# Kernel optimization log

Hardware: AMD Instinct MI355X
Metric: run time of the kernel (lower is better)

The kernel has to match this reference:

```python
import jax, jax.numpy as jnp
import numpy as np
from math import sqrt

D_MODEL = 1024
N_HEADS = 16
FF_MULT = 4
MAX_DIST = 512
LN_EPS = 1e-5


def layer_norm(x, g, b):
    mu = jnp.mean(x, axis=-1, keepdims=True)
    var = jnp.var(x, axis=-1, keepdims=True)
    return (x - mu) * jax.lax.rsqrt(var + LN_EPS) * g + b


def setup_inputs() -> dict:
    key = jax.random.key(0)
    ks = jax.random.split(key, 10)
    D, H, F = D_MODEL, N_HEADS, D_MODEL * FF_MULT
    s = 0.02
    return {
        "x": jax.random.normal(ks[0], (2, 2048, D), dtype=jnp.float32),
        "w_qkv": jax.random.normal(ks[1], (D, 3 * D), dtype=jnp.float32) * s,
        "b_qkv": jnp.zeros((3 * D,), jnp.float32),
        "w_out": jax.random.normal(ks[2], (D, D), dtype=jnp.float32) * s,
        "b_out": jnp.zeros((D,), jnp.float32),
        "rel_bias": jax.random.normal(ks[3], (2 * MAX_DIST + 1, H), dtype=jnp.float32) * s,
        "g1": jnp.ones((D,), jnp.float32),
        "beta1": jnp.zeros((D,), jnp.float32),
        "w1": jax.random.normal(ks[4], (D, F), dtype=jnp.float32) * s,
        "b1": jnp.zeros((F,), jnp.float32),
        "w2": jax.random.normal(ks[5], (F, D), dtype=jnp.float32) * s,
        "b2": jnp.zeros((D,), jnp.float32),
        "g2": jnp.ones((D,), jnp.float32),
        "beta2": jnp.zeros((D,), jnp.float32),
    }


def reference(x, w_qkv, b_qkv, w_out, b_out, rel_bias, g1, beta1, w1, b1, w2, b2, g2, beta2):
    B, T, D = x.shape
    H = N_HEADS
    hd = D // H
    qkv = x @ w_qkv + b_qkv                      # [B,T,3D]
    q, k, v = jnp.split(qkv, 3, axis=-1)
    # [B,H,T,hd]
    q = q.reshape(B, T, H, hd).transpose(0, 2, 1, 3)
    k = k.reshape(B, T, H, hd).transpose(0, 2, 1, 3)
    v = v.reshape(B, T, H, hd).transpose(0, 2, 1, 3)
    scores = jnp.einsum("bhqd,bhkd->bhqk", q, k) / sqrt(hd)
    # relative position bias: gather from table [2*max_dist+1, H]
    rel = jnp.clip(jnp.arange(T)[None, :] - jnp.arange(T)[:, None], -MAX_DIST, MAX_DIST) + MAX_DIST
    bias = rel_bias[rel].transpose(2, 0, 1)       # [H,T,T]
    attn = jax.nn.softmax(scores + bias[None], axis=-1)
    out = jnp.einsum("bhqk,bhkd->bhqd", attn, v).transpose(0, 2, 1, 3).reshape(B, T, D)
    out = out @ w_out + b_out                     # dropout inactive (eval)
    x2 = layer_norm(x + out, g1, beta1)
    ff = jax.nn.gelu(x2 @ w1 + b1, approximate=False) @ w2 + b2
    x3 = layer_norm(x2 + ff, g2, beta2)
    return (x3, attn)
```

## Files before the change

### kernel.cpp

```cpp
#include <hip/hip_runtime.h>
#include <hip/hip_bf16.h>
#include <cstdint>
#include <cstddef>

#define DEVFN static __device__ __forceinline__

typedef __attribute__((ext_vector_type(8))) short bf16x8;
typedef __attribute__((ext_vector_type(4))) float f32x4;

#define WAITVM(N) asm volatile("s_waitcnt vmcnt(" #N ")" ::: "memory")
#define WAITLGKM() asm volatile("s_waitcnt lgkmcnt(0)" ::: "memory")
#define BAR() __builtin_amdgcn_s_barrier()

DEVFN float exp2f_fast(float x) { return __builtin_amdgcn_exp2f(x); }

DEVFN ushort f2bf(float f) {
  uint32_t u = __float_as_uint(f);
  return (ushort)((u + 0x7fffu + ((u >> 16) & 1u)) >> 16);
}

DEVFN void gl_lds16(const void* g, void* l) {
  __builtin_amdgcn_global_load_lds(
      (const __attribute__((address_space(1))) void*)g,
      (__attribute__((address_space(3))) void*)l, 16, 0, 0);
}

DEVFN float wred_sum(float v) {
#pragma unroll
  for (int o = 32; o; o >>= 1) v += __shfl_xor(v, o);
  return v;
}


__global__ __launch_bounds__(256) void pack_bf16(const float* __restrict__ in,
                                                 ushort* __restrict__ out) {
  size_t i = ((size_t)blockIdx.x * 256 + threadIdx.x) * 4;
  float4 v = *(const float4*)&in[i];
  ushort4 u = make_ushort4(f2bf(v.x), f2bf(v.y), f2bf(v.z), f2bf(v.w));
  *(ushort4*)&out[i] = u;
}

__global__ __launch_bounds__(256) void wtrans(const float* __restrict__ in,
                                              ushort* __restrict__ out,
                                              int K, int N) {
  __shared__ float tile[32][33];
  int n0 = blockIdx.x * 32, k0 = blockIdx.y * 32;
  int tid = threadIdx.x;
#pragma unroll
  for (int i = 0; i < 4; ++i) {
    int idx = tid + i * 256;
    int r = idx >> 5, c = idx & 31;
    tile[r][c] = in[(size_t)(k0 + r) * N + n0 + c];
  }
  __syncthreads();
#pragma unroll
  for (int i = 0; i < 4; ++i) {
    int idx = tid + i * 256;
    int r = idx >> 5, c = idx & 31;
    out[(size_t)(n0 + r) * K + k0 + c] = f2bf(tile[c][r]);
  }
}

__global__ __launch_bounds__(256) void pack_vT(const ushort* __restrict__ qkv,
                                               ushort* __restrict__ vT) {
  __shared__ ushort tile[64][72];
  int bh = blockIdx.y, b = bh >> 4, h = bh & 15;
  int t0 = blockIdx.x * 64;
  int tid = threadIdx.x;
#pragma unroll
  for (int i = 0; i < 16; ++i) {
    int idx = tid + i * 256;
    int r = idx >> 6, c = idx & 63;
    tile[r][c] = qkv[(size_t)(b * 2048 + t0 + r) * 3072 + 2048 + h * 64 + c];
  }
  __syncthreads();
#pragma unroll
  for (int i = 0; i < 16; ++i) {
    int idx = tid + i * 256;
    int d = idx >> 6, t = idx & 63;
    vT[((size_t)bh * 64 + d) * 2048 + t0 + t] = tile[t][d];
  }
}


template <bool GELU, bool STF32, bool STBF16>
__global__ __launch_bounds__(256)
void gemm128(const ushort* __restrict__ A, int lda,
             const ushort* __restrict__ BT, int ldb,
             const float* __restrict__ bias,
             float* __restrict__ Cf, ushort* __restrict__ Cb, int ldc, int K) {
  __shared__ ushort lsa[128 * 64];
  __shared__ ushort lsb[128 * 64];
  const int tid = threadIdx.x;
  const int lane = tid & 63;
  const int wv = tid >> 6;
  const int wr = (wv >> 1) * 64, wc = (wv & 1) * 64;
  const ushort* Ab = A + (size_t)blockIdx.y * 128 * lda;
  const ushort* Bb = BT + (size_t)blockIdx.x * 128 * ldb;
  f32x4 acc[4][4] = {};
  int rowS[4], slotS[4];
#pragma unroll
  for (int i = 0; i < 4; ++i) {
    int idx = tid + i * 256;
    rowS[i] = idx >> 3;
    slotS[i] = (idx & 7) ^ (rowS[i] & 7);
  }
  for (int kt = 0; kt < K; kt += 64) {
    __syncthreads();
#pragma unroll
    for (int i = 0; i < 4; ++i) {
      gl_lds16(Ab + (size_t)rowS[i] * lda + kt + slotS[i] * 8, &lsa[(tid + i * 256) * 8]);
      gl_lds16(Bb + (size_t)rowS[i] * ldb + kt + slotS[i] * 8, &lsb[(tid + i * 256) * 8]);
    }
    asm volatile("s_waitcnt vmcnt(0)" ::: "memory");
    __syncthreads();
#pragma unroll
    for (int kk = 0; kk < 2; ++kk) {
      bf16x8 af[4], bfr[4];
      const int g = kk * 4 + (lane >> 4);
#pragma unroll
      for (int m = 0; m < 4; ++m) {
        int r = wr + m * 16 + (lane & 15);
        af[m] = *(const bf16x8*)&lsa[r * 64 + ((g ^ (r & 7)) * 8)];
      }
#pragma unroll
      for (int n = 0; n < 4; ++n) {
        int r = wc + n * 16 + (lane & 15);
        bfr[n] = *(const bf16x8*)&lsb[r * 64 + ((g ^ (r & 7)) * 8)];
      }
#pragma unroll
      for (int m = 0; m < 4; ++m)
#pragma unroll
        for (int n = 0; n < 4; ++n)
          acc[m][n] = __builtin_amdgcn_mfma_f32_16x16x32_bf16(af[m], bfr[n], acc[m][n], 0, 0, 0);
    }
  }
  const int rb = blockIdx.y * 128 + wr + ((lane >> 4) << 2);
  const int cb = blockIdx.x * 128 + wc + (lane & 15);
#pragma unroll
  for (int m = 0; m < 4; ++m)
#pragma unroll
    for (int n = 0; n < 4; ++n) {
      int col = cb + n * 16;
      float bv = bias[col];
#pragma unroll
      for (int i = 0; i < 4; ++i) {
        int row = rb + m * 16 + i;
        float v = acc[m][n][i] + bv;
        if (GELU) v = 0.5f * v * (1.0f + erff(v * 0.70710678f));
        if (STF32) Cf[(size_t)row * ldc + col] = v;
        if (STBF16) Cb[(size_t)row * ldc + col] = f2bf(v);
      }
    }
}


__global__ __launch_bounds__(256, 4)
void attn_den(const ushort* __restrict__ qkv, const float* __restrict__ rel_bias,
              float* __restrict__ invl) {
  __shared__ ushort lsk[2][64 * 64];
  __shared__ float extb[1034];
  const int tid = threadIdx.x;
  const int lane = tid & 63;
  const int wv = tid >> 6;
  const int hi = lane >> 4;
  const int lo = lane & 15;
  const int bh = blockIdx.y, b = bh >> 4, h = bh & 15;
  const int q0 = blockIdx.x * 128;
  const ushort* qp = qkv + (size_t)b * 2048 * 3072 + h * 64;
  const ushort* kp = qp + 1024;
  const float C_SC = 0.18033688011f;
  ushort* lsq = (ushort*)lsk;

  for (int i = tid; i < 1034; i += 256) {
    int j = i - 3;
    j = j < 0 ? 0 : (j > 1024 ? 1024 : j);
    extb[i] = rel_bias[j * 16 + h] * 1.44269504f;
  }
#pragma unroll
  for (int i = 0; i < 4; ++i) {
    int idx = tid + i * 256;
    int row = idx >> 3;
    int slot = (idx & 7) ^ (row & 7);
    gl_lds16(qp + (size_t)(q0 + row) * 3072 + slot * 8, &lsq[idx * 8]);
  }
  WAITVM(0);
  WAITLGKM();
  BAR();
  bf16x8 qf[2][2];
#pragma unroll
  for (int mq = 0; mq < 2; ++mq)
#pragma unroll
    for (int kk = 0; kk < 2; ++kk) {
      int r = wv * 32 + mq * 16 + lo;
      int g = kk * 4 + hi;
      qf[mq][kk] = *(const bf16x8*)&lsq[r * 64 + ((g ^ (r & 7)) * 8)];
    }
  WAITLGKM();
  BAR();

  const int r0 = tid >> 3;
  const int sl0 = (tid & 7) ^ (r0 & 7);
  const int r1 = (tid + 256) >> 3;
  const int sl1 = ((tid + 256) & 7) ^ (r1 & 7);
  auto stageK = [&](int t, int buf) {
    gl_lds16(kp + (size_t)(t * 64 + r0) * 3072 + sl0 * 8, &lsk[buf][tid * 8]);
    gl_lds16(kp + (size_t)(t * 64 + r1) * 3072 + sl1 * 8, &lsk[buf][(tid + 256) * 8]);
  };

  float l_part[2] = {0.0f, 0.0f};
  stageK(0, 0);
  for (int t = 0; t < 32; ++t) {
    if (t < 31) {
      stageK(t + 1, (t + 1) & 1);
      WAITVM(2);
    } else {
      WAITVM(0);
    }
    BAR();
    f32x4 sacc[4][2] = {};
    __builtin_amdgcn_s_setprio(1);
#pragma unroll
    for (int kk = 0; kk < 2; ++kk) {
      const int g = kk * 4 + hi;
      bf16x8 ak[4];
#pragma unroll
      for (int mk = 0; mk < 4; ++mk) {
        int r = mk * 16 + lo;
        ak[mk] = *(const bf16x8*)&lsk[t & 1][r * 64 + ((g ^ (r & 7)) * 8)];
      }
#pragma unroll
      for (int mk = 0; mk < 4; ++mk)
#pragma unroll
        for (int mq = 0; mq < 2; ++mq)
          sacc[mk][mq] =
              __builtin_amdgcn_mfma_f32_16x16x32_bf16(ak[mk], qf[mq][kk], sacc[mk][mq], 0, 0, 0);
    }
    __builtin_amdgcn_s_setprio(0);
    const bool farR = (t * 64) >= q0 + 640;
    const bool farL = (t * 64 + 63) <= q0 - 512;
    if (farR || farL) {
      const float bc = farR ? extb[3 + 1024] : extb[3];
#pragma unroll
      for (int mq = 0; mq < 2; ++mq) {
        float s = 0.0f;
#pragma unroll
        for (int mk = 0; mk < 4; ++mk)
#pragma unroll
          for (int i = 0; i < 4; ++i)
            s += exp2f_fast(fmaf(sacc[mk][mq][i], C_SC, bc));
        l_part[mq] += s;
      }
    } else {
      const int kbase = t * 64 + hi * 4;
      const int qr = q0 + wv * 32 + lo;
#pragma unroll
      for (int mq = 0; mq < 2; ++mq) {
        float s = 0.0f;
#pragma unroll
        for (int mk = 0; mk < 4; ++mk) {
          int k0 = (kbase + mk * 16) - (qr + mq * 16) + 515;
          k0 = k0 < 0 ? 0 : (k0 > 1030 ? 1030 : k0);
#pragma unroll
          for (int i = 0; i < 4; ++i)
            s += exp2f_fast(fmaf(sacc[mk][mq][i], C_SC, extb[k0 + i]));
        }
        l_part[mq] += s;
      }
    }
    BAR();
  }

#pragma unroll
  for (int mq = 0; mq < 2; ++mq) {
    float l = l_part[mq];
    l += __shfl_xor(l, 16);
    l += __shfl_xor(l, 32);
    if (hi == 0)
      invl[(size_t)bh * 2048 + q0 + wv * 32 + mq * 16 + lo] = 1.0f / l;
  }
}

__global__ __launch_bounds__(256, 3)
void attn_pv2(const ushort* __restrict__ qkv, const ushort* __restrict__ vT,
              const float* __restrict__ rel_bias, const float* __restrict__ invl,
              float* __restrict__ attn, ushort* __restrict__ ctx) {
  __shared__ ushort lsk[2][64 * 64];
  __shared__ ushort lsv[2][64 * 64];
  __shared__ ushort lsp[128 * 64];
  __shared__ float extb[1034];
  const int tid = threadIdx.x;
  const int lane = tid & 63;
  const int wv = tid >> 6;
  const int hi = lane >> 4;
  const int lo = lane & 15;
  const int bh = blockIdx.y, b = bh >> 4, h = bh & 15;
  const int q0 = blockIdx.x * 128;
  const ushort* qp = qkv + (size_t)b * 2048 * 3072 + h * 64;
  const ushort* kp = qp + 1024;
  const ushort* vp = vT + (size_t)bh * 64 * 2048;
  float* attnb = attn + (size_t)bh * 2048 * 2048;
  const float C_SC = 0.18033688011f;

  for (int i = tid; i < 1034; i += 256) {
    int j = i - 3;
    j = j < 0 ? 0 : (j > 1024 ? 1024 : j);
    extb[i] = rel_bias[j * 16 + h] * 1.44269504f;
  }
#pragma unroll
  for (int i = 0; i < 4; ++i) {
    int idx = tid + i * 256;
    int row = idx >> 3;
    int slot = (idx & 7) ^ (row & 7);
    gl_lds16(qp + (size_t)(q0 + row) * 3072 + slot * 8, &lsp[idx * 8]);
  }
  WAITVM(0);
  WAITLGKM();
  BAR();
  bf16x8 qf[2][2];
#pragma unroll
  for (int mq = 0; mq < 2; ++mq)
#pragma unroll
    for (int kk = 0; kk < 2; ++kk) {
      int r = wv * 32 + mq * 16 + lo;
      int g = kk * 4 + hi;
      qf[mq][kk] = *(const bf16x8*)&lsp[r * 64 + ((g ^ (r & 7)) * 8)];
    }
  WAITLGKM();
  BAR();

  float il[2];
#pragma unroll
  for (int mq = 0; mq < 2; ++mq)
    il[mq] = invl[(size_t)bh * 2048 + q0 + wv * 32 + mq * 16 + lo];

  const int r0 = tid >> 3;
  const int sl0 = (tid & 7) ^ (r0 & 7);
  const int r1 = (tid + 256) >> 3;
  const int sl1 = ((tid + 256) & 7) ^ (r1 & 7);
  auto stageK = [&](int t, int buf) {
    gl_lds16(kp + (size_t)(t * 64 + r0) * 3072 + sl0 * 8, &lsk[buf][tid * 8]);
    gl_lds16(kp + (size_t)(t * 64 + r1) * 3072 + sl1 * 8, &lsk[buf][(tid + 256) * 8]);
  };
  auto stageV = [&](int t, int buf) {
    gl_lds16(vp + (size_t)r0 * 2048 + t * 64 + sl0 * 8, &lsv[buf][tid * 8]);
    gl_lds16(vp + (size_t)r1 * 2048 + t * 64 + sl1 * 8, &lsv[buf][(tid + 256) * 8]);
  };

  f32x4 acc_o[2][4] = {};
  stageK(0, 0);
  stageV(0, 0);
  for (int t = 0; t < 32; ++t) {
    if (t < 31) {
      stageK(t + 1, (t + 1) & 1);
      stageV(t + 1, (t + 1) & 1);
    }
    if (t == 0) { WAITVM(4); }
    else if (t < 31) { WAITVM(12); }
    else { WAITVM(8); }
    BAR();
    f32x4 sacc[4][2] = {};
    __builtin_amdgcn_s_setprio(1);
#pragma unroll
    for (int kk = 0; kk < 2; ++kk) {
      const int g = kk * 4 + hi;
      bf16x8 ak[4];
#pragma unroll
      for (int mk = 0; mk < 4; ++mk) {
        int r = mk * 16 + lo;
        ak[mk] = *(const bf16x8*)&lsk[t & 1][r * 64 + ((g ^ (r & 7)) * 8)];
      }
#pragma unroll
      for (int mk = 0; mk < 4; ++mk)
#pragma unroll
        for (int mq = 0; mq < 2; ++mq)
          sacc[mk][mq] =
              __builtin_amdgcn_mfma_f32_16x16x32_bf16(ak[mk], qf[mq][kk], sacc[mk][mq], 0, 0, 0);
    }
    __builtin_amdgcn_s_setprio(0);
    const bool farR = (t * 64) >= q0 + 640;
    const bool farT = farR || ((t * 64 + 63) <= q0 - 512);
    const float bcf = farR ? extb[3 + 1024] : extb[3];
#pragma unroll
    for (int mq = 0; mq < 2; ++mq) {
      const int row = wv * 32 + mq * 16 + lo;
      const float l = il[mq];
#pragma unroll
      for (int mk = 0; mk < 4; ++mk) {
        const int c0 = mk * 16 + hi * 4;
        float p4[4];
        if (farT) {
#pragma unroll
          for (int i = 0; i < 4; ++i)
            p4[i] = exp2f_fast(fmaf(sacc[mk][mq][i], C_SC, bcf)) * l;
        } else {
          int k0 = (t * 64 + c0) - (q0 + row) + 515;
          k0 = k0 < 0 ? 0 : (k0 > 1030 ? 1030 : k0);
#pragma unroll
          for (int i = 0; i < 4; ++i)
            p4[i] = exp2f_fast(fmaf(sacc[mk][mq][i], C_SC, extb[k0 + i])) * l;
        }
        ushort4 u = make_ushort4(f2bf(p4[0]), f2bf(p4[1]), f2bf(p4[2]), f2bf(p4[3]));
        *(ushort4*)&lsp[row * 64 + (((c0 >> 3) ^ (row & 7)) << 3) + (c0 & 7)] = u;
        *(float4*)&attnb[(size_t)(q0 + row) * 2048 + t * 64 + c0] =
            make_float4(p4[0], p4[1], p4[2], p4[3]);
      }
    }
    WAITLGKM();
    BAR();
    __builtin_amdgcn_s_setprio(1);
#pragma unroll
    for (int kk = 0; kk < 2; ++kk) {
      const int g = kk * 4 + hi;
      bf16x8 ap[2], bv2[4];
#pragma unroll
      for (int m = 0; m < 2; ++m) {
        int r = wv * 32 + m * 16 + lo;
        ap[m] = *(const bf16x8*)&lsp[r * 64 + ((g ^ (r & 7)) * 8)];
      }
#pragma unroll
      for (int n = 0; n < 4; ++n) {
        int r = n * 16 + lo;
        bv2[n] = *(const bf16x8*)&lsv[t & 1][r * 64 + ((g ^ (r & 7)) * 8)];
      }
#pragma unroll
      for (int m = 0; m < 2; ++m)
#pragma unroll
        for (int n = 0; n < 4; ++n)
          acc_o[m][n] = __builtin_amdgcn_mfma_f32_16x16x32_bf16(ap[m], bv2[n], acc_o[m][n], 0, 0, 0);
    }
    __builtin_amdgcn_s_setprio(0);
  }

#pragma unroll
  for (int m = 0; m < 2; ++m)
#pragma unroll
    for (int n = 0; n < 4; ++n) {
      int col = h * 64 + n * 16 + lo;
#pragma unroll
      for (int i = 0; i < 4; ++i) {
        int row = q0 + wv * 32 + m * 16 + (hi << 2) + i;
        ctx[(size_t)(b * 2048 + row) * 1024 + col] = f2bf(acc_o[m][n][i]);
      }
    }
}


__global__ __launch_bounds__(256)
void add_ln(const float* __restrict__ a, const float* __restrict__ r,
            const float* __restrict__ g, const float* __restrict__ be,
            float* __restrict__ outf, ushort* __restrict__ outb) {
  const int tid = threadIdx.x;
  const size_t base = (size_t)blockIdx.x * 1024 + tid * 4;
  float4 va = *(const float4*)&a[base];
  float4 vr = *(const float4*)&r[base];
  float x0 = va.x + vr.x, x1 = va.y + vr.y, x2 = va.z + vr.z, x3 = va.w + vr.w;
  float s = x0 + x1 + x2 + x3;
  float s2 = x0 * x0 + x1 * x1 + x2 * x2 + x3 * x3;
  s = wred_sum(s);
  s2 = wred_sum(s2);
  __shared__ float rs[4], rq[4];
  if ((tid & 63) == 0) { rs[tid >> 6] = s; rq[tid >> 6] = s2; }
  __syncthreads();
  s = rs[0] + rs[1] + rs[2] + rs[3];
  s2 = rq[0] + rq[1] + rq[2] + rq[3];
  const float mean = s * (1.0f / 1024.0f);
  const float var = s2 * (1.0f / 1024.0f) - mean * mean;
  const float sc = rsqrtf(var + 1e-5f);
  float4 vg = *(const float4*)&g[tid * 4];
  float4 vb = *(const float4*)&be[tid * 4];
  float y0 = (x0 - mean) * sc * vg.x + vb.x;
  float y1 = (x1 - mean) * sc * vg.y + vb.y;
  float y2 = (x2 - mean) * sc * vg.z + vb.z;
  float y3 = (x3 - mean) * sc * vg.w + vb.w;
  *(float4*)&outf[base] = make_float4(y0, y1, y2, y3);
  if (outb) {
    ushort4 u = make_ushort4(f2bf(y0), f2bf(y1), f2bf(y2), f2bf(y3));
    *(ushort4*)&outb[base] = u;
  }
}


extern "C" void kernel_launch(void* const* d_in, const int* in_sizes, int n_in,
                              void* d_out, int out_size, void* d_ws, size_t ws_size,
                              hipStream_t stream) {
  const float* x     = (const float*)d_in[0];
  const float* w_qkv = (const float*)d_in[1];
  const float* b_qkv = (const float*)d_in[2];
  const float* w_out = (const float*)d_in[3];
  const float* b_out = (const float*)d_in[4];
  const float* relb  = (const float*)d_in[5];
  const float* g1    = (const float*)d_in[6];
  const float* be1   = (const float*)d_in[7];
  const float* w1    = (const float*)d_in[8];
  const float* b1    = (const float*)d_in[9];
  const float* w2    = (const float*)d_in[10];
  const float* b2    = (const float*)d_in[11];
  const float* g2    = (const float*)d_in[12];
  const float* be2   = (const float*)d_in[13];

  float* x3o  = (float*)d_out;
  float* attn = x3o + (size_t)4194304;

  char* w = (char*)d_ws;
  size_t off = 0;
  auto alloc = [&](size_t bytes) {
    void* p = w + off;
    off += (bytes + 255) & ~(size_t)255;
    return p;
  };
  ushort* x_bf   = (ushort*)alloc(4096ull * 1024 * 2);
  ushort* wqkvT  = (ushort*)alloc(3072ull * 1024 * 2);
  ushort* woutT  = (ushort*)alloc(1024ull * 1024 * 2);
  ushort* w1T    = (ushort*)alloc(4096ull * 1024 * 2);
  ushort* w2T    = (ushort*)alloc(1024ull * 4096 * 2);
  ushort* qkv_bf = (ushort*)alloc(4096ull * 3072 * 2);
  ushort* vT     = (ushort*)alloc(32ull * 64 * 2048 * 2);
  ushort* ctx_bf = (ushort*)alloc(4096ull * 1024 * 2);
  float*  invl   = (float*)alloc(32ull * 2048 * 4);
  float*  projf  = (float*)alloc(4096ull * 1024 * 4);
  float*  x2f    = (float*)alloc(4096ull * 1024 * 4);
  ushort* x2bf   = (ushort*)alloc(4096ull * 1024 * 2);
  ushort* ff1_bf = (ushort*)alloc(4096ull * 4096 * 2);
  float*  ff2f   = projf;

  pack_bf16<<<4096, 256, 0, stream>>>(x, x_bf);
  wtrans<<<dim3(96, 32), 256, 0, stream>>>(w_qkv, wqkvT, 1024, 3072);
  wtrans<<<dim3(32, 32), 256, 0, stream>>>(w_out, woutT, 1024, 1024);
  wtrans<<<dim3(128, 32), 256, 0, stream>>>(w1, w1T, 1024, 4096);
  wtrans<<<dim3(32, 128), 256, 0, stream>>>(w2, w2T, 4096, 1024);

  gemm128<false, false, true><<<dim3(24, 32), 256, 0, stream>>>(
      x_bf, 1024, wqkvT, 1024, b_qkv, nullptr, qkv_bf, 3072, 1024);
  attn_den<<<dim3(16, 32), 256, 0, stream>>>(qkv_bf, relb, invl);
  pack_vT<<<dim3(32, 32), 256, 0, stream>>>(qkv_bf, vT);
  attn_pv2<<<dim3(16, 32), 256, 0, stream>>>(qkv_bf, vT, relb, invl, attn, ctx_bf);

  gemm128<false, true, false><<<dim3(8, 32), 256, 0, stream>>>(
      ctx_bf, 1024, woutT, 1024, b_out, projf, nullptr, 1024, 1024);
  add_ln<<<4096, 256, 0, stream>>>(x, projf, g1, be1, x2f, x2bf);
  gemm128<true, false, true><<<dim3(32, 32), 256, 0, stream>>>(
      x2bf, 1024, w1T, 1024, b1, nullptr, ff1_bf, 4096, 1024);
  gemm128<false, true, false><<<dim3(8, 32), 256, 0, stream>>>(
      ff1_bf, 4096, w2T, 4096, b2, ff2f, nullptr, 1024, 4096);
  add_ln<<<4096, 256, 0, stream>>>(x2f, ff2f, g2, be2, x3o, nullptr);
}
```

Before: 511.1 us.

## Split-K the N=1024 GEMMs and remap attention blocks for XCD locality

The output-projection and FF2 GEMMs now use a two-way split-K over a third grid dimension, writing two fp32 partials. The following add+LayerNorm kernel sums both partials and adds the bias, which the GEMM no longer applies. This doubles the block count of the 256-block GEMMs to fill the GPU, at the cost of an extra fp32 partial buffer write and read. The attention kernels also switch to a 1D grid whose block IDs are remapped so blocks of the same head land on the same XCD, aiming to improve L2 reuse of K/V.

```diff
diff --git a/kernel.cpp b/kernel.cpp
--- a/kernel.cpp
+++ b/kernel.cpp
@@ -88,15 +88,17 @@
 void gemm128(const ushort* __restrict__ A, int lda,
              const ushort* __restrict__ BT, int ldb,
              const float* __restrict__ bias,
-             float* __restrict__ Cf, ushort* __restrict__ Cb, int ldc, int K) {
+             float* __restrict__ Cf, ushort* __restrict__ Cb, int ldc, int K,
+             size_t cstride) {
   __shared__ ushort lsa[128 * 64];
   __shared__ ushort lsb[128 * 64];
   const int tid = threadIdx.x;
   const int lane = tid & 63;
   const int wv = tid >> 6;
   const int wr = (wv >> 1) * 64, wc = (wv & 1) * 64;
-  const ushort* Ab = A + (size_t)blockIdx.y * 128 * lda;
-  const ushort* Bb = BT + (size_t)blockIdx.x * 128 * ldb;
+  const size_t kStart = (size_t)blockIdx.z * K;
+  const ushort* Ab = A + (size_t)blockIdx.y * 128 * lda + kStart;
+  const ushort* Bb = BT + (size_t)blockIdx.x * 128 * ldb + kStart;
   f32x4 acc[4][4] = {};
   int rowS[4], slotS[4];
 #pragma unroll
@@ -137,23 +139,34 @@
   }
   const int rb = blockIdx.y * 128 + wr + ((lane >> 4) << 2);
   const int cb = blockIdx.x * 128 + wc + (lane & 15);
+  float* Cfz = Cf + (size_t)blockIdx.z * cstride;
+  ushort* Cbz = Cb + (size_t)blockIdx.z * cstride;
 #pragma unroll
   for (int m = 0; m < 4; ++m)
 #pragma unroll
     for (int n = 0; n < 4; ++n) {
       int col = cb + n * 16;
-      float bv = bias[col];
+      float bv = bias ? bias[col] : 0.0f;
 #pragma unroll
       for (int i = 0; i < 4; ++i) {
         int row = rb + m * 16 + i;
         float v = acc[m][n][i] + bv;
         if (GELU) v = 0.5f * v * (1.0f + erff(v * 0.70710678f));
-        if (STF32) Cf[(size_t)row * ldc + col] = v;
-        if (STBF16) Cb[(size_t)row * ldc + col] = f2bf(v);
-      }
-    }
-}
-
+        if (STF32) Cfz[(size_t)row * ldc + col] = v;
+        if (STBF16) Cbz[(size_t)row * ldc + col] = f2bf(v);
+      }
+    }
+}
+
+
+DEVFN void attn_bid(int& qb, int& bh) {
+  int lin = blockIdx.x;
+  int xcd = lin & 7;
+  int idx = lin >> 3;
+  int orig = xcd * 64 + idx;
+  qb = orig & 15;
+  bh = orig >> 4;
+}
 
 __global__ __launch_bounds__(256, 4)
 void attn_den(const ushort* __restrict__ qkv, const float* __restrict__ rel_bias,
@@ -165,8 +178,10 @@
   const int wv = tid >> 6;
   const int hi = lane >> 4;
   const int lo = lane & 15;
-  const int bh = blockIdx.y, b = bh >> 4, h = bh & 15;
-  const int q0 = blockIdx.x * 128;
+  int qb, bh;
+  attn_bid(qb, bh);
+  const int b = bh >> 4, h = bh & 15;
+  const int q0 = qb * 128;
   const ushort* qp = qkv + (size_t)b * 2048 * 3072 + h * 64;
   const ushort* kp = qp + 1024;
   const float C_SC = 0.18033688011f;
@@ -294,8 +309,10 @@
   const int wv = tid >> 6;
   const int hi = lane >> 4;
   const int lo = lane & 15;
-  const int bh = blockIdx.y, b = bh >> 4, h = bh & 15;
-  const int q0 = blockIdx.x * 128;
+  int qb, bh;
+  attn_bid(qb, bh);
+  const int b = bh >> 4, h = bh & 15;
+  const int q0 = qb * 128;
   const ushort* qp = qkv + (size_t)b * 2048 * 3072 + h * 64;
   const ushort* kp = qp + 1024;
   const ushort* vp = vT + (size_t)bh * 64 * 2048;
@@ -447,14 +464,23 @@
 
 
 __global__ __launch_bounds__(256)
-void add_ln(const float* __restrict__ a, const float* __restrict__ r,
+void add_ln(const float* __restrict__ a, const float* __restrict__ r0,
+            const float* __restrict__ r1, const float* __restrict__ bias,
             const float* __restrict__ g, const float* __restrict__ be,
             float* __restrict__ outf, ushort* __restrict__ outb) {
   const int tid = threadIdx.x;
   const size_t base = (size_t)blockIdx.x * 1024 + tid * 4;
   float4 va = *(const float4*)&a[base];
-  float4 vr = *(const float4*)&r[base];
+  float4 vr = *(const float4*)&r0[base];
   float x0 = va.x + vr.x, x1 = va.y + vr.y, x2 = va.z + vr.z, x3 = va.w + vr.w;
+  if (r1) {
+    float4 v1 = *(const float4*)&r1[base];
+    x0 += v1.x; x1 += v1.y; x2 += v1.z; x3 += v1.w;
+  }
+  if (bias) {
+    float4 vb4 = *(const float4*)&bias[tid * 4];
+    x0 += vb4.x; x1 += vb4.y; x2 += vb4.z; x3 += vb4.w;
+  }
   float s = x0 + x1 + x2 + x3;
   float s2 = x0 * x0 + x1 * x1 + x2 * x2 + x3 * x3;
   s = wred_sum(s);
@@ -518,11 +544,11 @@
   ushort* vT     = (ushort*)alloc(32ull * 64 * 2048 * 2);
   ushort* ctx_bf = (ushort*)alloc(4096ull * 1024 * 2);
   float*  invl   = (float*)alloc(32ull * 2048 * 4);
-  float*  projf  = (float*)alloc(4096ull * 1024 * 4);
+  float*  p0     = (float*)alloc(4096ull * 1024 * 4);
+  float*  p1     = (float*)alloc(4096ull * 1024 * 4);
   float*  x2f    = (float*)alloc(4096ull * 1024 * 4);
   ushort* x2bf   = (ushort*)alloc(4096ull * 1024 * 2);
   ushort* ff1_bf = (ushort*)alloc(4096ull * 4096 * 2);
-  float*  ff2f   = projf;
 
   pack_bf16<<<4096, 256, 0, stream>>>(x, x_bf);
   wtrans<<<dim3(96, 32), 256, 0, stream>>>(w_qkv, wqkvT, 1024, 3072);
@@ -531,17 +557,19 @@
   wtrans<<<dim3(32, 128), 256, 0, stream>>>(w2, w2T, 4096, 1024);
 
   gemm128<false, false, true><<<dim3(24, 32), 256, 0, stream>>>(
-      x_bf, 1024, wqkvT, 1024, b_qkv, nullptr, qkv_bf, 3072, 1024);
-  attn_den<<<dim3(16, 32), 256, 0, stream>>>(qkv_bf, relb, invl);
+      x_bf, 1024, wqkvT, 1024, b_qkv, nullptr, qkv_bf, 3072, 1024, 0);
+  attn_den<<<512, 256, 0, stream>>>(qkv_bf, relb, invl);
   pack_vT<<<dim3(32, 32), 256, 0, stream>>>(qkv_bf, vT);
-  attn_pv2<<<dim3(16, 32), 256, 0, stream>>>(qkv_bf, vT, relb, invl, attn, ctx_bf);
-
-  gemm128<false, true, false><<<dim3(8, 32), 256, 0, stream>>>(
-      ctx_bf, 1024, woutT, 1024, b_out, projf, nullptr, 1024, 1024);
-  add_ln<<<4096, 256, 0, stream>>>(x, projf, g1, be1, x2f, x2bf);
+  attn_pv2<<<512, 256, 0, stream>>>(qkv_bf, vT, relb, invl, attn, ctx_bf);
+
+  gemm128<false, true, false><<<dim3(8, 32, 2), 256, 0, stream>>>(
+      ctx_bf, 1024, woutT, 1024, nullptr, p0, nullptr, 1024, 512,
+      (size_t)(p1 - p0));
+  add_ln<<<4096, 256, 0, stream>>>(x, p0, p1, b_out, g1, be1, x2f, x2bf);
   gemm128<true, false, true><<<dim3(32, 32), 256, 0, stream>>>(
-      x2bf, 1024, w1T, 1024, b1, nullptr, ff1_bf, 4096, 1024);
-  gemm128<false, true, false><<<dim3(8, 32), 256, 0, stream>>>(
-      ff1_bf, 4096, w2T, 4096, b2, ff2f, nullptr, 1024, 4096);
-  add_ln<<<4096, 256, 0, stream>>>(x2f, ff2f, g2, be2, x3o, nullptr);
-}
+      x2bf, 1024, w1T, 1024, b1, nullptr, ff1_bf, 4096, 1024, 0);
+  gemm128<false, true, false><<<dim3(8, 32, 2), 256, 0, stream>>>(
+      ff1_bf, 4096, w2T, 4096, nullptr, p0, nullptr, 1024, 2048,
+      (size_t)(p1 - p0));
+  add_ln<<<4096, 256, 0, stream>>>(x2f, p0, p1, b2, g2, be2, x3o, nullptr);
+}
```

New measurement: 452.0 us. -11.6%, faster.
